# Kernel optimization log

Measured on AMD Instinct MI355X. Metric: run time of the kernel, lower is better.

The kernel has to match this reference:

```python
import jax, jax.numpy as jnp
import numpy as np

D = 18          # belief dimension (max category dim)
EPS = 0.1       # C.eps
PROP_STEP = 5   # C.prop_step
CC = 0.01       # label-injection constant c in forward
DIM_A = 4       # category_dim_dict['author']
DIM_P = 18      # category_dim_dict['paper']


def _init_belief(mask, label, dim, d):
    # X[tr_idx] = -c everywhere, then X[tr_idx, label] += dim*c
    m = (mask != 0).astype(jnp.float32)[:, None]            # [N,1]
    X = -CC * m + (dim * CC) * m * jax.nn.one_hot(label, d, dtype=jnp.float32)
    col_mask = (jnp.arange(d) < dim).astype(jnp.float32)    # zero cols >= dim
    Y = X * col_mask
    return X, Y, col_mask


def setup_inputs() -> dict:
    key = jax.random.key(0)
    ks = jax.random.split(key, 8)
    E, NA, NP = 2_000_000, 100_000, 500_000
    return {
        "H_ap": jax.random.normal(ks[0], (D, D), dtype=jnp.float32),
        "H_pa": jax.random.normal(ks[1], (D, D), dtype=jnp.float32),
        "w": jnp.ones((E,), dtype=jnp.float32),
        "edge_src": jax.random.randint(ks[2], (E,), 0, NA, dtype=jnp.int32),
        "edge_dst": jax.random.randint(ks[3], (E,), 0, NP, dtype=jnp.int32),
        "train_mask_a": jax.random.randint(ks[4], (NA,), 0, 2, dtype=jnp.int32),
        "label_a": jax.random.randint(ks[5], (NA,), 0, DIM_A, dtype=jnp.int32),
        "train_mask_p": jax.random.randint(ks[6], (NP,), 0, 2, dtype=jnp.int32),
        "label_p": jax.random.randint(ks[7], (NP,), 0, DIM_P, dtype=jnp.int32),
        "n_author": NA,
        "n_paper": NP,
    }


def reference(H_ap, H_pa, w, edge_src, edge_dst, train_mask_a, label_a,
              train_mask_p, label_p, n_author, n_paper):
    # Belief init via scatter-based label injection (per node type)
    Xa, Ya, cm_a = _init_belief(train_mask_a, label_a, DIM_A, D)
    Xp, Yp, cm_p = _init_belief(train_mask_p, label_p, DIM_P, D)

    seg = jax.ops.segment_sum
    for _ in range(PROP_STEP):  # ZooBP residual updates over hetero edge types
        # author -> paper: gather, transform by H_ap, weighted scatter-add
        msg_p = seg(w[:, None] * (Ya[edge_src] @ H_ap), edge_dst,
                    num_segments=n_paper)                       # [NP, D]
        # paper -> author (inverse etype, H_pa ~ H_ap^T structure)
        msg_a = seg(w[:, None] * (Yp[edge_dst] @ H_pa), edge_src,
                    num_segments=n_author)                      # [NA, D]
        Ya = (Xa + (EPS / D) * msg_a) * cm_a
        Yp = (Xp + (EPS / D) * msg_p) * cm_p
    return Ya, Yp
```

## Files before the change

### kernel.cpp

```cpp
#include <hip/hip_runtime.h>


static constexpr int   DD     = 18;
static constexpr int   DIMA   = 4;
static constexpr float CCF    = 0.01f;
static constexpr float SCALEF = 0.1f / 18.0f;
static constexpr int   PROP   = 5;

static constexpr int NBLK  = 512;
static constexpr int PSH   = 11;
static constexpr int ASH   = 9;
static constexpr int PBK   = 256;
static constexpr int ABK   = 256;
static constexpr int PNB   = 1 << PSH;
static constexpr int ANB   = 1 << ASH;
static constexpr int NBIN  = PBK + ABK;
static constexpr int NBINS = NBIN * NBLK;

__device__ __forceinline__ float bf2f(unsigned short u) {
    return __uint_as_float(((unsigned int)u) << 16);
}
__device__ __forceinline__ unsigned short f2bf(float f) {
    unsigned int x = __float_as_uint(f);
    return (unsigned short)((x + 0x7fffu + ((x >> 16) & 1u)) >> 16);
}
__device__ __forceinline__ unsigned int f2w13(float f) {
    unsigned int x = __float_as_uint(f);
    return ((x + 0x3ffffu + ((x >> 19) & 1u)) >> 19) & 0x1fffu;
}
__device__ __forceinline__ float w132f(unsigned int u) {
    return __uint_as_float(u << 19);
}
__device__ __forceinline__ int swz_blk() {
    return ((int)blockIdx.x & 7) * (NBLK >> 3) + ((int)blockIdx.x >> 3);
}

__global__ __launch_bounds__(256) void count_bins(
    const int* __restrict__ esrc, const int* __restrict__ edst,
    int* __restrict__ bb, int E, int chunk)
{
    __shared__ int hP[PBK];
    __shared__ int hA[ABK];
    int t = threadIdx.x, b = swz_blk();
    if (t < PBK) hP[t] = 0;
    if (t < ABK) hA[t] = 0;
    __syncthreads();
    int beg = b * chunk;
    int end = beg + chunk; if (end > E) end = E;
    for (int e = beg + t; e < end; e += 256) {
        atomicAdd(&hP[edst[e] >> PSH], 1);
        atomicAdd(&hA[esrc[e] >> ASH], 1);
    }
    __syncthreads();
    if (t < PBK) bb[t * NBLK + b] = hP[t];
    if (t < ABK) bb[(PBK + t) * NBLK + b] = hA[t];
}

__global__ __launch_bounds__(256) void scan_block(
    int* __restrict__ off, int* __restrict__ bsum, int NT)
{
    __shared__ int s[256];
    int t = threadIdx.x;
    int i = blockIdx.x * 256 + t;
    int v = (i < NT) ? off[i] : 0;
    s[t] = v; __syncthreads();
    for (int dlt = 1; dlt < 256; dlt <<= 1) {
        int x = (t >= dlt) ? s[t - dlt] : 0;
        __syncthreads();
        s[t] += x;
        __syncthreads();
    }
    if (i < NT) off[i] = s[t] - v;
    if (t == 255) bsum[blockIdx.x] = s[255];
}

__global__ __launch_bounds__(256) void scan_tops(int* __restrict__ bsum, int nb)
{
    __shared__ int s[256];
    int t = threadIdx.x;
    int K = (nb + 255) / 256;
    int base = t * K;
    int sum = 0;
    for (int r = 0; r < K; ++r) { int idx = base + r; if (idx < nb) sum += bsum[idx]; }
    s[t] = sum; __syncthreads();
    for (int dlt = 1; dlt < 256; dlt <<= 1) {
        int x = (t >= dlt) ? s[t - dlt] : 0;
        __syncthreads();
        s[t] += x;
        __syncthreads();
    }
    int run = s[t] - sum;
    for (int r = 0; r < K; ++r) {
        int idx = base + r;
        if (idx < nb) { int tmp = bsum[idx]; bsum[idx] = run; run += tmp; }
    }
}

__global__ __launch_bounds__(256) void scat_p(
    const int* __restrict__ esrc, const int* __restrict__ edst,
    const float* __restrict__ w, const int* __restrict__ bb,
    const int* __restrict__ bsum, uint2* __restrict__ S, int E, int chunk)
{
    __shared__ int base[PBK];
    int t = threadIdx.x, b = swz_blk();
    if (t < PBK) {
        int idx = t * NBLK + b;
        base[t] = bb[idx] + bsum[idx >> 8];
    }
    __syncthreads();
    int beg = b * chunk;
    int end = beg + chunk; if (end > E) end = E;
    for (int e = beg + t; e < end; e += 256) {
        int d = edst[e], s = esrc[e];
        unsigned int rec = ((unsigned int)s << 13) | f2w13(w[e]);
        int pos = atomicAdd(&base[d >> PSH], 1);
        S[pos] = make_uint2(rec, (unsigned int)(d & (PNB - 1)));
    }
}

__global__ __launch_bounds__(256) void scat_a(
    const int* __restrict__ esrc, const int* __restrict__ edst,
    const float* __restrict__ w, const int* __restrict__ bb,
    const int* __restrict__ bsum, uint2* __restrict__ S, int E, int chunk)
{
    __shared__ int base[ABK];
    int t = threadIdx.x, b = swz_blk();
    if (t < ABK) {
        int idx = (PBK + t) * NBLK + b;
        base[t] = bb[idx] + bsum[idx >> 8] - E;
    }
    __syncthreads();
    int beg = b * chunk;
    int end = beg + chunk; if (end > E) end = E;
    for (int e = beg + t; e < end; e += 256) {
        int d = edst[e], s = esrc[e];
        unsigned int rec = ((unsigned int)d << 13) | f2w13(w[e]);
        int pos = atomicAdd(&base[s >> ASH], 1);
        S[pos] = make_uint2(rec, (unsigned int)(s & (ANB - 1)));
    }
}

__global__ __launch_bounds__(256) void csr_p(
    const int* __restrict__ bb, const int* __restrict__ bsum,
    const uint2* __restrict__ S,
    unsigned int* __restrict__ adjP, int* __restrict__ offP, int NP, int E)
{
    __shared__ int c[PNB];
    __shared__ int loc[PNB];
    __shared__ int ps[256];
    int t = threadIdx.x, b = blockIdx.x;
    int i0 = b * NBLK;
    int i1 = (b + 1) * NBLK;
    int sbeg = bb[i0] + bsum[i0 >> 8];
    int send = bb[i1] + bsum[i1 >> 8];
    for (int i = t; i < PNB; i += 256) c[i] = 0;
    __syncthreads();
    for (int i = sbeg + t; i < send; i += 256)
        atomicAdd(&c[S[i].y], 1);
    __syncthreads();
    int a[8]; int sum = 0;
#pragma unroll
    for (int k = 0; k < 8; ++k) { a[k] = c[t * 8 + k]; sum += a[k]; }
    ps[t] = sum; __syncthreads();
    for (int dlt = 1; dlt < 256; dlt <<= 1) {
        int x = (t >= dlt) ? ps[t - dlt] : 0;
        __syncthreads();
        ps[t] += x;
        __syncthreads();
    }
    int run = ps[t] - sum;
    int n0 = (b << PSH) + t * 8;
#pragma unroll
    for (int k = 0; k < 8; ++k) {
        loc[t * 8 + k] = run;
        if (n0 + k < NP) offP[n0 + k] = sbeg + run;
        run += a[k];
    }
    if (b == 0 && t == 0) offP[NP] = E;
    __syncthreads();
    for (int i = sbeg + t; i < send; i += 256) {
        uint2 r = S[i];
        int p = atomicAdd(&loc[r.y], 1);
        adjP[sbeg + p] = r.x;
    }
}

__global__ __launch_bounds__(256) void csr_a(
    const int* __restrict__ bb, const int* __restrict__ bsum,
    const uint2* __restrict__ S,
    unsigned int* __restrict__ adjA, int* __restrict__ offA, int NA, int E)
{
    __shared__ int c[ANB];
    __shared__ int loc[ANB];
    __shared__ int ps[256];
    int t = threadIdx.x, b = blockIdx.x;
    int x0 = (PBK + b) * NBLK;
    int sbeg = bb[x0] + bsum[x0 >> 8] - E;
    int send;
    if (b == ABK - 1) send = E;
    else { int x1 = x0 + NBLK; send = bb[x1] + bsum[x1 >> 8] - E; }
    c[t] = 0; c[t + 256] = 0;
    __syncthreads();
    for (int i = sbeg + t; i < send; i += 256)
        atomicAdd(&c[S[i].y], 1);
    __syncthreads();
    int a0 = c[2 * t], a1 = c[2 * t + 1];
    ps[t] = a0 + a1;
    __syncthreads();
    for (int dlt = 1; dlt < 256; dlt <<= 1) {
        int x = (t >= dlt) ? ps[t - dlt] : 0;
        __syncthreads();
        ps[t] += x;
        __syncthreads();
    }
    int ex = ps[t] - a0 - a1;
    loc[2 * t] = ex;
    loc[2 * t + 1] = ex + a0;
    int n0 = (b << ASH) + 2 * t;
    if (n0 < NA)     offA[n0]     = sbeg + ex;
    if (n0 + 1 < NA) offA[n0 + 1] = sbeg + ex + a0;
    if (b == 0 && t == 0) offA[NA] = E;
    __syncthreads();
    for (int i = sbeg + t; i < send; i += 256) {
        uint2 r = S[i];
        int p = atomicAdd(&loc[r.y], 1);
        adjA[sbeg + p] = r.x;
    }
}

__global__ __launch_bounds__(256) void init_belief(
    const int* __restrict__ mask_a, const int* __restrict__ lab_a,
    const int* __restrict__ mask_p, const int* __restrict__ lab_p,
    const float* __restrict__ Hpa,
    ushort4* __restrict__ Ya, ushort4* __restrict__ Zp,
    unsigned char* __restrict__ priorA, unsigned char* __restrict__ priorP,
    int NA, int NT)
{
    __shared__ float sH[72], sCol[4];
    int t = threadIdx.x;
    if (t < 72) sH[t] = Hpa[(t >> 2) * DD + (t & 3)];
    if (t < 4) { float s = 0.f; for (int k = 0; k < DD; ++k) s += Hpa[k * DD + t]; sCol[t] = s; }
    __syncthreads();
    int i = (int)blockIdx.x * 256 + t;
    if (i >= NT) return;
    if (i < NA) {
        float x[4] = {0.f, 0.f, 0.f, 0.f};
        int m = mask_a[i];
        int l = m ? lab_a[i] : 0;
        if (m) {
            x[0] = x[1] = x[2] = x[3] = -CCF;
            x[l] += (float)DIMA * CCF;
        }
        priorA[i] = m ? (unsigned char)(0x20 | l) : 0;
        Ya[i] = make_ushort4(f2bf(x[0]), f2bf(x[1]), f2bf(x[2]), f2bf(x[3]));
    } else {
        int d = i - NA;
        float z0 = 0.f, z1 = 0.f, z2 = 0.f, z3 = 0.f;
        int m = mask_p[d];
        int l = m ? lab_p[d] : 0;
        if (m) {
            float lb = (float)DD * CCF;
            z0 = -CCF * sCol[0] + lb * sH[l * 4 + 0];
            z1 = -CCF * sCol[1] + lb * sH[l * 4 + 1];
            z2 = -CCF * sCol[2] + lb * sH[l * 4 + 2];
            z3 = -CCF * sCol[3] + lb * sH[l * 4 + 3];
        }
        priorP[d] = m ? (unsigned char)(0x20 | l) : 0;
        Zp[d] = make_ushort4(f2bf(z0), f2bf(z1), f2bf(z2), f2bf(z3));
    }
}

__global__ __launch_bounds__(256) void gather_iter(
    const int* __restrict__ offP, const int* __restrict__ offA,
    const unsigned int* __restrict__ adjP, const unsigned int* __restrict__ adjA,
    const ushort4* __restrict__ ZpOld, ushort4* __restrict__ ZpNew,
    const ushort4* __restrict__ YaOld, ushort4* __restrict__ YaNew,
    const unsigned char* __restrict__ priorA, const unsigned char* __restrict__ priorP,
    const float* __restrict__ Hap, const float* __restrict__ Hpa,
    float* __restrict__ out, int NP, int NA, int last, int gpB)
{
    if ((int)blockIdx.x < gpB) {
        __shared__ float sH[72], sCol[4], sM[16], sHap[72];
        int t = threadIdx.x;
        if (t < 72) sH[t] = Hpa[(t >> 2) * DD + (t & 3)];
        if (t < 4) { float s = 0.f; for (int k = 0; k < DD; ++k) s += Hpa[k * DD + t]; sCol[t] = s; }
        if (t < 16) { int i = t >> 2, j = t & 3; float s = 0.f;
                      for (int k = 0; k < DD; ++k) s += Hap[i * DD + k] * Hpa[k * DD + j];
                      sM[t] = SCALEF * s; }
        if (t < 72) sHap[t] = SCALEF * Hap[t];
        __syncthreads();

        int d = (int)blockIdx.x * 256 + t;
        if (d >= NP) return;
        int beg = offP[d], end = offP[d + 1];
        float ax = 0.f, ay = 0.f, az = 0.f, aw = 0.f;
        int s = beg;
        for (; s + 4 <= end; s += 4) {
            unsigned int e0 = adjP[s], e1 = adjP[s + 1], e2 = adjP[s + 2], e3 = adjP[s + 3];
            ushort4 y0 = YaOld[e0 >> 13], y1 = YaOld[e1 >> 13];
            ushort4 y2 = YaOld[e2 >> 13], y3 = YaOld[e3 >> 13];
            float w0 = w132f(e0 & 0x1fffu), w1 = w132f(e1 & 0x1fffu);
            float w2 = w132f(e2 & 0x1fffu), w3 = w132f(e3 & 0x1fffu);
            ax += w0 * bf2f(y0.x) + w1 * bf2f(y1.x) + w2 * bf2f(y2.x) + w3 * bf2f(y3.x);
            ay += w0 * bf2f(y0.y) + w1 * bf2f(y1.y) + w2 * bf2f(y2.y) + w3 * bf2f(y3.y);
            az += w0 * bf2f(y0.z) + w1 * bf2f(y1.z) + w2 * bf2f(y2.z) + w3 * bf2f(y3.z);
            aw += w0 * bf2f(y0.w) + w1 * bf2f(y1.w) + w2 * bf2f(y2.w) + w3 * bf2f(y3.w);
        }
        for (; s < end; ++s) {
            unsigned int ent = adjP[s];
            float wt = w132f(ent & 0x1fffu);
            ushort4 yv = YaOld[ent >> 13];
            ax += wt * bf2f(yv.x); ay += wt * bf2f(yv.y);
            az += wt * bf2f(yv.z); aw += wt * bf2f(yv.w);
        }
        unsigned int pb = priorP[d];
        int l = pb & 31;
        float base = pb ? -CCF : 0.f;
        float lb   = pb ? (float)DD * CCF : 0.f;
        float z0 = base * sCol[0] + lb * sH[l * 4 + 0] + ax * sM[0] + ay * sM[4] + az * sM[8]  + aw * sM[12];
        float z1 = base * sCol[1] + lb * sH[l * 4 + 1] + ax * sM[1] + ay * sM[5] + az * sM[9]  + aw * sM[13];
        float z2 = base * sCol[2] + lb * sH[l * 4 + 2] + ax * sM[2] + ay * sM[6] + az * sM[10] + aw * sM[14];
        float z3 = base * sCol[3] + lb * sH[l * 4 + 3] + ax * sM[3] + ay * sM[7] + az * sM[11] + aw * sM[15];
        ZpNew[d] = make_ushort4(f2bf(z0), f2bf(z1), f2bf(z2), f2bf(z3));

        if (last) {
            float* row = out + (size_t)(NA + d) * DD;
#pragma unroll
            for (int j = 0; j < DD; ++j) {
                row[j] = base + ((j == l) ? lb : 0.f)
                       + ax * sHap[0 * DD + j] + ay * sHap[1 * DD + j]
                       + az * sHap[2 * DD + j] + aw * sHap[3 * DD + j];
            }
        }
    } else {
        int tid = ((int)blockIdx.x - gpB) * 256 + threadIdx.x;
        int a = tid >> 2, sub = tid & 3;
        if (a >= NA) return;
        int beg = offA[a], end = offA[a + 1];
        float ax = 0.f, ay = 0.f, az = 0.f, aw = 0.f;
        int s = beg + sub;
        for (; s + 12 < end; s += 16) {
            unsigned int e0 = adjA[s], e1 = adjA[s + 4], e2 = adjA[s + 8], e3 = adjA[s + 12];
            ushort4 z0 = ZpOld[e0 >> 13], z1 = ZpOld[e1 >> 13];
            ushort4 z2 = ZpOld[e2 >> 13], z3 = ZpOld[e3 >> 13];
            float w0 = w132f(e0 & 0x1fffu), w1 = w132f(e1 & 0x1fffu);
            float w2 = w132f(e2 & 0x1fffu), w3 = w132f(e3 & 0x1fffu);
            ax += w0 * bf2f(z0.x) + w1 * bf2f(z1.x) + w2 * bf2f(z2.x) + w3 * bf2f(z3.x);
            ay += w0 * bf2f(z0.y) + w1 * bf2f(z1.y) + w2 * bf2f(z2.y) + w3 * bf2f(z3.y);
            az += w0 * bf2f(z0.z) + w1 * bf2f(z1.z) + w2 * bf2f(z2.z) + w3 * bf2f(z3.z);
            aw += w0 * bf2f(z0.w) + w1 * bf2f(z1.w) + w2 * bf2f(z2.w) + w3 * bf2f(z3.w);
        }
        for (; s < end; s += 4) {
            unsigned int ent = adjA[s];
            float wt = w132f(ent & 0x1fffu);
            ushort4 z = ZpOld[ent >> 13];
            ax += wt * bf2f(z.x); ay += wt * bf2f(z.y);
            az += wt * bf2f(z.z); aw += wt * bf2f(z.w);
        }
        ax += __shfl_xor(ax, 1); ay += __shfl_xor(ay, 1);
        az += __shfl_xor(az, 1); aw += __shfl_xor(aw, 1);
        ax += __shfl_xor(ax, 2); ay += __shfl_xor(ay, 2);
        az += __shfl_xor(az, 2); aw += __shfl_xor(aw, 2);
        if (sub == 0) {
            unsigned int pb = priorA[a];
            int l = pb & 31;
            float x0 = pb ? ((l == 0) ? ((float)DIMA - 1.f) * CCF : -CCF) : 0.f;
            float x1 = pb ? ((l == 1) ? ((float)DIMA - 1.f) * CCF : -CCF) : 0.f;
            float x2 = pb ? ((l == 2) ? ((float)DIMA - 1.f) * CCF : -CCF) : 0.f;
            float x3 = pb ? ((l == 3) ? ((float)DIMA - 1.f) * CCF : -CCF) : 0.f;
            float y0 = x0 + SCALEF * ax, y1 = x1 + SCALEF * ay;
            float y2 = x2 + SCALEF * az, y3 = x3 + SCALEF * aw;
            YaNew[a] = make_ushort4(f2bf(y0), f2bf(y1), f2bf(y2), f2bf(y3));
            if (last) {
                float* row = out + (size_t)a * DD;
                row[0] = y0; row[1] = y1; row[2] = y2; row[3] = y3;
#pragma unroll
                for (int j = DIMA; j < DD; ++j) row[j] = 0.f;
            }
        }
    }
}

extern "C" void kernel_launch(void* const* d_in, const int* in_sizes, int n_in,
                              void* d_out, int out_size, void* d_ws, size_t ws_size,
                              hipStream_t stream)
{
    const float* H_ap   = (const float*)d_in[0];
    const float* H_pa   = (const float*)d_in[1];
    const float* w      = (const float*)d_in[2];
    const int*   esrc   = (const int*)d_in[3];
    const int*   edst   = (const int*)d_in[4];
    const int*   mask_a = (const int*)d_in[5];
    const int*   lab_a  = (const int*)d_in[6];
    const int*   mask_p = (const int*)d_in[7];
    const int*   lab_p  = (const int*)d_in[8];

    const int E  = in_sizes[2];
    const int NA = in_sizes[5];
    const int NP = in_sizes[7];
    const int NT = NP + NA;

    char*  basep = (char*)d_ws;
    size_t o = 0;
    auto alloc = [&](size_t bytes) -> char* {
        o = (o + 15) & ~(size_t)15;
        char* p = basep + o;
        o += bytes;
        return p;
    };
    int*           offP   = (int*)          alloc((size_t)(NP + 1) * sizeof(int));
    int*           offA   = (int*)          alloc((size_t)(NA + 1) * sizeof(int));
    int*           bb     = (int*)          alloc((size_t)(NBINS + 1) * sizeof(int));
    int*           bsum   = (int*)          alloc((size_t)4096 * sizeof(int));
    unsigned int*  adjP   = (unsigned int*) alloc((size_t)E * sizeof(unsigned int));
    unsigned int*  adjA   = (unsigned int*) alloc((size_t)E * sizeof(unsigned int));
    unsigned char* priorP = (unsigned char*)alloc((size_t)NP);
    unsigned char* priorA = (unsigned char*)alloc((size_t)NA);
    size_t s_bytes  = (size_t)E * sizeof(uint2);
    size_t bl_bytes = (size_t)(2 * NA + 2 * NP) * sizeof(ushort4);
    char*  Sreg = alloc(s_bytes > bl_bytes ? s_bytes : bl_bytes);
    uint2* S    = (uint2*)Sreg;
    ushort4* YaA = (ushort4*)Sreg;
    ushort4* YaB = YaA + NA;
    ushort4* ZpA = YaB + NA;
    ushort4* ZpB = ZpA + NP;
    (void)ws_size;

    float* out = (float*)d_out;
    ushort4* YaBuf[2] = {YaA, YaB};
    ushort4* ZpBuf[2] = {ZpA, ZpB};

    dim3 blk(256);
    const int chunk = (E + NBLK - 1) / NBLK;
    const int gp    = (NP + 255) / 256;
    const int ga4   = (NA * 4 + 255) / 256;
    const int gni   = (NT + 255) / 256;
    const int nb    = (NBINS + 255) / 256;

    count_bins<<<NBLK, blk, 0, stream>>>(esrc, edst, bb, E, chunk);
    scan_block<<<nb, blk, 0, stream>>>(bb, bsum, NBINS);
    scan_tops<<<1, blk, 0, stream>>>(bsum, nb);
    scat_p<<<NBLK, blk, 0, stream>>>(esrc, edst, w, bb, bsum, S, E, chunk);
    csr_p<<<PBK, blk, 0, stream>>>(bb, bsum, S, adjP, offP, NP, E);
    scat_a<<<NBLK, blk, 0, stream>>>(esrc, edst, w, bb, bsum, S, E, chunk);
    csr_a<<<ABK, blk, 0, stream>>>(bb, bsum, S, adjA, offA, NA, E);
    init_belief<<<gni, blk, 0, stream>>>(mask_a, lab_a, mask_p, lab_p, H_pa,
                                         YaA, ZpA, priorA, priorP, NA, NT);

    for (int it = 0; it < PROP; ++it) {
        int last = (it == PROP - 1) ? 1 : 0;
        int cur = it & 1, nxt = 1 - cur;
        gather_iter<<<gp + ga4, blk, 0, stream>>>(offP, offA, adjP, adjA,
                                                  ZpBuf[cur], ZpBuf[nxt],
                                                  YaBuf[cur], YaBuf[nxt],
                                                  priorA, priorP,
                                                  H_ap, H_pa, out,
                                                  NP, NA, last, gp);
    }
}
```

Measured before the change: 372.3 us.

## Add nontemporal loads/stores and fuse CSR-author build with belief init

```diff
diff --git a/kernel.cpp b/kernel.cpp
--- a/kernel.cpp
+++ b/kernel.cpp
@@ -31,6 +31,18 @@
 __device__ __forceinline__ float w132f(unsigned int u) {
     return __uint_as_float(u << 19);
 }
+__device__ __forceinline__ int          nt_i32(const int* p)          { return __builtin_nontemporal_load(p); }
+__device__ __forceinline__ unsigned int nt_u32(const unsigned int* p) { return __builtin_nontemporal_load(p); }
+__device__ __forceinline__ float        nt_f32(const float* p)        { return __builtin_nontemporal_load(p); }
+__device__ __forceinline__ void nt_store_us4(ushort4* p, ushort4 v) {
+    unsigned long long x = (unsigned long long)v.x | ((unsigned long long)v.y << 16)
+                         | ((unsigned long long)v.z << 32) | ((unsigned long long)v.w << 48);
+    __builtin_nontemporal_store(x, (unsigned long long*)p);
+}
+__device__ __forceinline__ void nt_store_u2(uint2* p, uint2 v) {
+    unsigned long long x = (unsigned long long)v.x | ((unsigned long long)v.y << 32);
+    __builtin_nontemporal_store(x, (unsigned long long*)p);
+}
 __device__ __forceinline__ int swz_blk() {
     return ((int)blockIdx.x & 7) * (NBLK >> 3) + ((int)blockIdx.x >> 3);
 }
@@ -48,8 +60,8 @@
     int beg = b * chunk;
     int end = beg + chunk; if (end > E) end = E;
     for (int e = beg + t; e < end; e += 256) {
-        atomicAdd(&hP[edst[e] >> PSH], 1);
-        atomicAdd(&hA[esrc[e] >> ASH], 1);
+        atomicAdd(&hP[nt_i32(edst + e) >> PSH], 1);
+        atomicAdd(&hA[nt_i32(esrc + e) >> ASH], 1);
     }
     __syncthreads();
     if (t < PBK) bb[t * NBLK + b] = hP[t];
@@ -111,10 +123,10 @@
     int beg = b * chunk;
     int end = beg + chunk; if (end > E) end = E;
     for (int e = beg + t; e < end; e += 256) {
-        int d = edst[e], s = esrc[e];
-        unsigned int rec = ((unsigned int)s << 13) | f2w13(w[e]);
+        int d = nt_i32(edst + e), s = nt_i32(esrc + e);
+        unsigned int rec = ((unsigned int)s << 13) | f2w13(nt_f32(w + e));
         int pos = atomicAdd(&base[d >> PSH], 1);
-        S[pos] = make_uint2(rec, (unsigned int)(d & (PNB - 1)));
+        nt_store_u2(S + pos, make_uint2(rec, (unsigned int)(d & (PNB - 1))));
     }
 }
 
@@ -133,10 +145,10 @@
     int beg = b * chunk;
     int end = beg + chunk; if (end > E) end = E;
     for (int e = beg + t; e < end; e += 256) {
-        int d = edst[e], s = esrc[e];
-        unsigned int rec = ((unsigned int)d << 13) | f2w13(w[e]);
+        int d = nt_i32(edst + e), s = nt_i32(esrc + e);
+        unsigned int rec = ((unsigned int)d << 13) | f2w13(nt_f32(w + e));
         int pos = atomicAdd(&base[s >> ASH], 1);
-        S[pos] = make_uint2(rec, (unsigned int)(s & (ANB - 1)));
+        nt_store_u2(S + pos, make_uint2(rec, (unsigned int)(s & (ANB - 1))));
     }
 }
 
@@ -185,88 +197,87 @@
     }
 }
 
-__global__ __launch_bounds__(256) void csr_a(
+__global__ __launch_bounds__(256) void csr_a_init(
     const int* __restrict__ bb, const int* __restrict__ bsum,
     const uint2* __restrict__ S,
-    unsigned int* __restrict__ adjA, int* __restrict__ offA, int NA, int E)
-{
-    __shared__ int c[ANB];
-    __shared__ int loc[ANB];
-    __shared__ int ps[256];
-    int t = threadIdx.x, b = blockIdx.x;
-    int x0 = (PBK + b) * NBLK;
-    int sbeg = bb[x0] + bsum[x0 >> 8] - E;
-    int send;
-    if (b == ABK - 1) send = E;
-    else { int x1 = x0 + NBLK; send = bb[x1] + bsum[x1 >> 8] - E; }
-    c[t] = 0; c[t + 256] = 0;
-    __syncthreads();
-    for (int i = sbeg + t; i < send; i += 256)
-        atomicAdd(&c[S[i].y], 1);
-    __syncthreads();
-    int a0 = c[2 * t], a1 = c[2 * t + 1];
-    ps[t] = a0 + a1;
-    __syncthreads();
-    for (int dlt = 1; dlt < 256; dlt <<= 1) {
-        int x = (t >= dlt) ? ps[t - dlt] : 0;
-        __syncthreads();
-        ps[t] += x;
-        __syncthreads();
-    }
-    int ex = ps[t] - a0 - a1;
-    loc[2 * t] = ex;
-    loc[2 * t + 1] = ex + a0;
-    int n0 = (b << ASH) + 2 * t;
-    if (n0 < NA)     offA[n0]     = sbeg + ex;
-    if (n0 + 1 < NA) offA[n0 + 1] = sbeg + ex + a0;
-    if (b == 0 && t == 0) offA[NA] = E;
-    __syncthreads();
-    for (int i = sbeg + t; i < send; i += 256) {
-        uint2 r = S[i];
-        int p = atomicAdd(&loc[r.y], 1);
-        adjA[sbeg + p] = r.x;
-    }
-}
-
-__global__ __launch_bounds__(256) void init_belief(
+    unsigned int* __restrict__ adjA, int* __restrict__ offA,
     const int* __restrict__ mask_a, const int* __restrict__ lab_a,
     const int* __restrict__ mask_p, const int* __restrict__ lab_p,
     const float* __restrict__ Hpa,
     ushort4* __restrict__ Ya, ushort4* __restrict__ Zp,
     unsigned char* __restrict__ priorA, unsigned char* __restrict__ priorP,
-    int NA, int NT)
-{
-    __shared__ float sH[72], sCol[4];
-    int t = threadIdx.x;
-    if (t < 72) sH[t] = Hpa[(t >> 2) * DD + (t & 3)];
-    if (t < 4) { float s = 0.f; for (int k = 0; k < DD; ++k) s += Hpa[k * DD + t]; sCol[t] = s; }
-    __syncthreads();
-    int i = (int)blockIdx.x * 256 + t;
-    if (i >= NT) return;
-    if (i < NA) {
-        float x[4] = {0.f, 0.f, 0.f, 0.f};
-        int m = mask_a[i];
-        int l = m ? lab_a[i] : 0;
-        if (m) {
-            x[0] = x[1] = x[2] = x[3] = -CCF;
-            x[l] += (float)DIMA * CCF;
-        }
-        priorA[i] = m ? (unsigned char)(0x20 | l) : 0;
-        Ya[i] = make_ushort4(f2bf(x[0]), f2bf(x[1]), f2bf(x[2]), f2bf(x[3]));
+    int NA, int NTot, int E)
+{
+    if ((int)blockIdx.x < ABK) {
+        __shared__ int c[ANB];
+        __shared__ int loc[ANB];
+        __shared__ int ps[256];
+        int t = threadIdx.x, b = blockIdx.x;
+        int x0 = (PBK + b) * NBLK;
+        int sbeg = bb[x0] + bsum[x0 >> 8] - E;
+        int send;
+        if (b == ABK - 1) send = E;
+        else { int x1 = x0 + NBLK; send = bb[x1] + bsum[x1 >> 8] - E; }
+        c[t] = 0; c[t + 256] = 0;
+        __syncthreads();
+        for (int i = sbeg + t; i < send; i += 256)
+            atomicAdd(&c[S[i].y], 1);
+        __syncthreads();
+        int a0 = c[2 * t], a1 = c[2 * t + 1];
+        ps[t] = a0 + a1;
+        __syncthreads();
+        for (int dlt = 1; dlt < 256; dlt <<= 1) {
+            int x = (t >= dlt) ? ps[t - dlt] : 0;
+            __syncthreads();
+            ps[t] += x;
+            __syncthreads();
+        }
+        int ex = ps[t] - a0 - a1;
+        loc[2 * t] = ex;
+        loc[2 * t + 1] = ex + a0;
+        int n0 = (b << ASH) + 2 * t;
+        if (n0 < NA)     offA[n0]     = sbeg + ex;
+        if (n0 + 1 < NA) offA[n0 + 1] = sbeg + ex + a0;
+        if (b == 0 && t == 0) offA[NA] = E;
+        __syncthreads();
+        for (int i = sbeg + t; i < send; i += 256) {
+            uint2 r = S[i];
+            int p = atomicAdd(&loc[r.y], 1);
+            adjA[sbeg + p] = r.x;
+        }
     } else {
-        int d = i - NA;
-        float z0 = 0.f, z1 = 0.f, z2 = 0.f, z3 = 0.f;
-        int m = mask_p[d];
-        int l = m ? lab_p[d] : 0;
-        if (m) {
-            float lb = (float)DD * CCF;
-            z0 = -CCF * sCol[0] + lb * sH[l * 4 + 0];
-            z1 = -CCF * sCol[1] + lb * sH[l * 4 + 1];
-            z2 = -CCF * sCol[2] + lb * sH[l * 4 + 2];
-            z3 = -CCF * sCol[3] + lb * sH[l * 4 + 3];
-        }
-        priorP[d] = m ? (unsigned char)(0x20 | l) : 0;
-        Zp[d] = make_ushort4(f2bf(z0), f2bf(z1), f2bf(z2), f2bf(z3));
+        __shared__ float sH[72], sCol[4];
+        int t = threadIdx.x;
+        if (t < 72) sH[t] = Hpa[(t >> 2) * DD + (t & 3)];
+        if (t < 4) { float s = 0.f; for (int k = 0; k < DD; ++k) s += Hpa[k * DD + t]; sCol[t] = s; }
+        __syncthreads();
+        int i = ((int)blockIdx.x - ABK) * 256 + t;
+        if (i >= NTot) return;
+        if (i < NA) {
+            float x[4] = {0.f, 0.f, 0.f, 0.f};
+            int m = mask_a[i];
+            int l = m ? lab_a[i] : 0;
+            if (m) {
+                x[0] = x[1] = x[2] = x[3] = -CCF;
+                x[l] += (float)DIMA * CCF;
+            }
+            priorA[i] = m ? (unsigned char)(0x20 | l) : 0;
+            Ya[i] = make_ushort4(f2bf(x[0]), f2bf(x[1]), f2bf(x[2]), f2bf(x[3]));
+        } else {
+            int d = i - NA;
+            float z0 = 0.f, z1 = 0.f, z2 = 0.f, z3 = 0.f;
+            int m = mask_p[d];
+            int l = m ? lab_p[d] : 0;
+            if (m) {
+                float lb = (float)DD * CCF;
+                z0 = -CCF * sCol[0] + lb * sH[l * 4 + 0];
+                z1 = -CCF * sCol[1] + lb * sH[l * 4 + 1];
+                z2 = -CCF * sCol[2] + lb * sH[l * 4 + 2];
+                z3 = -CCF * sCol[3] + lb * sH[l * 4 + 3];
+            }
+            priorP[d] = m ? (unsigned char)(0x20 | l) : 0;
+            Zp[d] = make_ushort4(f2bf(z0), f2bf(z1), f2bf(z2), f2bf(z3));
+        }
     }
 }
 
@@ -292,11 +303,12 @@
 
         int d = (int)blockIdx.x * 256 + t;
         if (d >= NP) return;
-        int beg = offP[d], end = offP[d + 1];
+        int beg = nt_i32(offP + d), end = nt_i32(offP + d + 1);
         float ax = 0.f, ay = 0.f, az = 0.f, aw = 0.f;
         int s = beg;
         for (; s + 4 <= end; s += 4) {
-            unsigned int e0 = adjP[s], e1 = adjP[s + 1], e2 = adjP[s + 2], e3 = adjP[s + 3];
+            unsigned int e0 = nt_u32(adjP + s),     e1 = nt_u32(adjP + s + 1);
+            unsigned int e2 = nt_u32(adjP + s + 2), e3 = nt_u32(adjP + s + 3);
             ushort4 y0 = YaOld[e0 >> 13], y1 = YaOld[e1 >> 13];
             ushort4 y2 = YaOld[e2 >> 13], y3 = YaOld[e3 >> 13];
             float w0 = w132f(e0 & 0x1fffu), w1 = w132f(e1 & 0x1fffu);
@@ -307,7 +319,7 @@
             aw += w0 * bf2f(y0.w) + w1 * bf2f(y1.w) + w2 * bf2f(y2.w) + w3 * bf2f(y3.w);
         }
         for (; s < end; ++s) {
-            unsigned int ent = adjP[s];
+            unsigned int ent = nt_u32(adjP + s);
             float wt = w132f(ent & 0x1fffu);
             ushort4 yv = YaOld[ent >> 13];
             ax += wt * bf2f(yv.x); ay += wt * bf2f(yv.y);
@@ -321,26 +333,28 @@
         float z1 = base * sCol[1] + lb * sH[l * 4 + 1] + ax * sM[1] + ay * sM[5] + az * sM[9]  + aw * sM[13];
         float z2 = base * sCol[2] + lb * sH[l * 4 + 2] + ax * sM[2] + ay * sM[6] + az * sM[10] + aw * sM[14];
         float z3 = base * sCol[3] + lb * sH[l * 4 + 3] + ax * sM[3] + ay * sM[7] + az * sM[11] + aw * sM[15];
-        ZpNew[d] = make_ushort4(f2bf(z0), f2bf(z1), f2bf(z2), f2bf(z3));
+        nt_store_us4(ZpNew + d, make_ushort4(f2bf(z0), f2bf(z1), f2bf(z2), f2bf(z3)));
 
         if (last) {
             float* row = out + (size_t)(NA + d) * DD;
 #pragma unroll
             for (int j = 0; j < DD; ++j) {
-                row[j] = base + ((j == l) ? lb : 0.f)
-                       + ax * sHap[0 * DD + j] + ay * sHap[1 * DD + j]
-                       + az * sHap[2 * DD + j] + aw * sHap[3 * DD + j];
+                float v = base + ((j == l) ? lb : 0.f)
+                        + ax * sHap[0 * DD + j] + ay * sHap[1 * DD + j]
+                        + az * sHap[2 * DD + j] + aw * sHap[3 * DD + j];
+                __builtin_nontemporal_store(v, row + j);
             }
         }
     } else {
         int tid = ((int)blockIdx.x - gpB) * 256 + threadIdx.x;
         int a = tid >> 2, sub = tid & 3;
         if (a >= NA) return;
-        int beg = offA[a], end = offA[a + 1];
+        int beg = nt_i32(offA + a), end = nt_i32(offA + a + 1);
         float ax = 0.f, ay = 0.f, az = 0.f, aw = 0.f;
         int s = beg + sub;
         for (; s + 12 < end; s += 16) {
-            unsigned int e0 = adjA[s], e1 = adjA[s + 4], e2 = adjA[s + 8], e3 = adjA[s + 12];
+            unsigned int e0 = nt_u32(adjA + s),     e1 = nt_u32(adjA + s + 4);
+            unsigned int e2 = nt_u32(adjA + s + 8), e3 = nt_u32(adjA + s + 12);
             ushort4 z0 = ZpOld[e0 >> 13], z1 = ZpOld[e1 >> 13];
             ushort4 z2 = ZpOld[e2 >> 13], z3 = ZpOld[e3 >> 13];
             float w0 = w132f(e0 & 0x1fffu), w1 = w132f(e1 & 0x1fffu);
@@ -351,7 +365,7 @@
             aw += w0 * bf2f(z0.w) + w1 * bf2f(z1.w) + w2 * bf2f(z2.w) + w3 * bf2f(z3.w);
         }
         for (; s < end; s += 4) {
-            unsigned int ent = adjA[s];
+            unsigned int ent = nt_u32(adjA + s);
             float wt = w132f(ent & 0x1fffu);
             ushort4 z = ZpOld[ent >> 13];
             ax += wt * bf2f(z.x); ay += wt * bf2f(z.y);
@@ -370,12 +384,16 @@
             float x3 = pb ? ((l == 3) ? ((float)DIMA - 1.f) * CCF : -CCF) : 0.f;
             float y0 = x0 + SCALEF * ax, y1 = x1 + SCALEF * ay;
             float y2 = x2 + SCALEF * az, y3 = x3 + SCALEF * aw;
-            YaNew[a] = make_ushort4(f2bf(y0), f2bf(y1), f2bf(y2), f2bf(y3));
+            nt_store_us4(YaNew + a, make_ushort4(f2bf(y0), f2bf(y1), f2bf(y2), f2bf(y3)));
             if (last) {
                 float* row = out + (size_t)a * DD;
-                row[0] = y0; row[1] = y1; row[2] = y2; row[3] = y3;
+                __builtin_nontemporal_store(y0, row + 0);
+                __builtin_nontemporal_store(y1, row + 1);
+                __builtin_nontemporal_store(y2, row + 2);
+                __builtin_nontemporal_store(y3, row + 3);
 #pragma unroll
-                for (int j = DIMA; j < DD; ++j) row[j] = 0.f;
+                for (int j = DIMA; j < DD; ++j)
+                    __builtin_nontemporal_store(0.f, row + j);
             }
         }
     }
@@ -416,14 +434,11 @@
     unsigned int*  adjA   = (unsigned int*) alloc((size_t)E * sizeof(unsigned int));
     unsigned char* priorP = (unsigned char*)alloc((size_t)NP);
     unsigned char* priorA = (unsigned char*)alloc((size_t)NA);
-    size_t s_bytes  = (size_t)E * sizeof(uint2);
-    size_t bl_bytes = (size_t)(2 * NA + 2 * NP) * sizeof(ushort4);
-    char*  Sreg = alloc(s_bytes > bl_bytes ? s_bytes : bl_bytes);
-    uint2* S    = (uint2*)Sreg;
-    ushort4* YaA = (ushort4*)Sreg;
-    ushort4* YaB = YaA + NA;
-    ushort4* ZpA = YaB + NA;
-    ushort4* ZpB = ZpA + NP;
+    uint2*         S      = (uint2*)        alloc((size_t)E * sizeof(uint2));
+    ushort4*       YaA    = (ushort4*)      alloc((size_t)NA * sizeof(ushort4));
+    ushort4*       YaB    = (ushort4*)      alloc((size_t)NA * sizeof(ushort4));
+    ushort4*       ZpA    = (ushort4*)      alloc((size_t)NP * sizeof(ushort4));
+    ushort4*       ZpB    = (ushort4*)S;
     (void)ws_size;
 
     float* out = (float*)d_out;
@@ -443,9 +458,10 @@
     scat_p<<<NBLK, blk, 0, stream>>>(esrc, edst, w, bb, bsum, S, E, chunk);
     csr_p<<<PBK, blk, 0, stream>>>(bb, bsum, S, adjP, offP, NP, E);
     scat_a<<<NBLK, blk, 0, stream>>>(esrc, edst, w, bb, bsum, S, E, chunk);
-    csr_a<<<ABK, blk, 0, stream>>>(bb, bsum, S, adjA, offA, NA, E);
-    init_belief<<<gni, blk, 0, stream>>>(mask_a, lab_a, mask_p, lab_p, H_pa,
-                                         YaA, ZpA, priorA, priorP, NA, NT);
+    csr_a_init<<<ABK + gni, blk, 0, stream>>>(bb, bsum, S, adjA, offA,
+                                              mask_a, lab_a, mask_p, lab_p, H_pa,
+                                              YaA, ZpA, priorA, priorP,
+                                              NA, NT, E);
 
     for (int it = 0; it < PROP; ++it) {
         int last = (it == PROP - 1) ? 1 : 0;
```

Measured after the change: 502.4 us. +35.0%, slower.
